# Performance work log

Hardware: AMD Instinct MI355X
Metric: run time of the kernel (lower is better)

## Reference

```python
import jax, jax.numpy as jnp
import numpy as np
import math

EPS = 1e-6
KP = -1.0  # Poincare ball curvature (c=1 -> kappa=-1)
KS = 1.0   # stereographic sphere projection (c=1 -> kappa=+1)

def _n(x):
    return jnp.sqrt(jnp.sum(x * x, -1, keepdims=True) + 1e-15)

def tan_k(u, k):
    if k < 0:
        return jnp.tanh(u)
    return jnp.tan(jnp.clip(u, -1.47079, 1.47079))

def artan_k(u, k):
    if k < 0:
        return jnp.arctanh(jnp.clip(u, -1 + 1e-5, 1 - 1e-5))
    return jnp.arctan(u)

def proj(x, k):
    if k < 0:
        n = _n(x)
        m = 1.0 - 1e-4
        return jnp.where(n > m, x * (m / n), x)
    return x

def expmap0(u, k):
    n = _n(u)
    return proj(tan_k(n, k) * u / n, k)

def logmap0(y, k):
    n = _n(y)
    return artan_k(n, k) * y / n

def _safe_den(d):
    return jnp.where(d >= 0, jnp.maximum(d, EPS), jnp.minimum(d, -EPS))

def mobius_add(x, y, k):
    x2 = jnp.sum(x * x, -1, keepdims=True)
    y2 = jnp.sum(y * y, -1, keepdims=True)
    xy = jnp.sum(x * y, -1, keepdims=True)
    num = (1 - 2 * k * xy - k * y2) * x + (1 + k * x2) * y
    den = 1 - 2 * k * xy + k * k * x2 * y2
    return proj(num / _safe_den(den), k)

def mobius_pw_mul(w, x, k):
    wx = w * x
    nx = _n(x)
    nwx = _n(wx)
    return proj(tan_k(nwx / nx * artan_k(nx, k), k) * wx / nwx, k)

def mobius_smul(r, x, k):
    n = _n(x)
    return proj(tan_k(r * artan_k(n, k), k) * x / n, k)

def wmid(xs, k, axis, w=None):
    lam = 2.0 / (1.0 + k * jnp.sum(xs * xs, -1, keepdims=True))
    if w is None:
        w = jnp.ones_like(lam)
    num = jnp.sum(w * lam * xs, axis=axis)
    den = jnp.abs(jnp.sum(w * (lam - 1.0), axis=axis))
    return mobius_smul(0.5, num / jnp.maximum(den, EPS), k)

def slin(x, W, b, k=None):
    if k is None:
        return x @ W.T + b
    return expmap0(logmap0(x, k) @ W.T + b, k)

def dist(x, y, k):
    return 2.0 * artan_k(_n(mobius_add(-x, y, k))[..., 0], k)

def hyp_attn(kk, q, v, k):
    # kk, v: [N,K,h]; q: [N,h]
    sc = -dist(q[:, None, :], kk, k)              # [N,K]
    a = jax.nn.softmax(sc, axis=1)[..., None]
    return wmid(v, k, axis=1, w=a)

def euc_attn(kk, q, v):
    sc = jnp.einsum('nkh,nh->nk', kk, q) / math.sqrt(kk.shape[-1])
    a = jax.nn.softmax(sc, axis=1)
    return jnp.einsum('nk,nkh->nh', a, v)


def _forward(x, h1, c1, h2, c2, h3, c3, del_t, iou1, iou2, iou3,
             Wq_w, Wq_b, Wc_w, Wc_b, Uf_w, Uf_b, Up_w, Up_b,
             Uiou_w, Uiou_b, d, nbr):
    sg, th = jax.nn.sigmoid, jnp.tanh
    # mailbox gather (message_func + DGL mailbox), [N,K,h]
    mh1, mh2, mh3 = h1[nbr], h2[nbr], h3[nbr]
    mc1, mc2, mc3 = c1[nbr], c2[nbr], c3[nbr]
    g_t = (d / (del_t[nbr] + 1.0))[..., None]      # [N,K,1]

    x_1p = slin(expmap0(x, KP), Wq_w, Wq_b, KP)
    x_1s = slin(expmap0(x, KS), Wq_w, Wq_b, KS)
    x_1e = slin(x, Wq_w, Wq_b)

    s1 = logmap0(sg(slin(mh1, Up_w, Up_b, KP)), KP)
    s2 = logmap0(sg(slin(mh2, Up_w, Up_b, KS)), KS)
    s3 = sg(slin(mh3, Up_w, Up_b))

    ht1p = mobius_pw_mul(s1, mh1, KP)
    ht2p = mobius_pw_mul(s2, expmap0(logmap0(mh2, KS), KP), KP)
    ht3p = mobius_pw_mul(s3, expmap0(mh3, KP), KP)
    h_1p = 3.0 * wmid(jnp.stack([ht1p, ht2p, ht3p]), KP, axis=0)

    ht1s = mobius_pw_mul(s1, expmap0(logmap0(mh1, KP), KS), KP)
    ht2s = mobius_pw_mul(s2, mh2, KS)
    ht3s = mobius_pw_mul(s3, expmap0(mh3, KS), KS)
    h_1s = 3.0 * wmid(jnp.stack([ht1s, ht2s, ht3s]), KP, axis=0)

    ht1e = logmap0(mobius_pw_mul(s1, mh1, KP), KP)
    ht2e = logmap0(mobius_pw_mul(s2, mh2, KS), KS)
    h_1e = ht1e + ht2e + s3 * mh3

    h_tildp = hyp_attn(h_1p, x_1p, h_1p, KP)
    h_tilds = hyp_attn(h_1s, x_1s, h_1s, KS)
    h_tilde = euc_attn(h_1e, x_1e, h_1e)

    # Poincare cell path
    csk_p = expmap0(th(logmap0(slin(mc1, Wc_w, Wc_b, KP), KP)), KP)
    ckt_p = mobius_add(mobius_add(-csk_p, mc1, KP), mobius_pw_mul(csk_p, g_t, KP), KP)
    f_p = sg(logmap0(slin(mh1, Uf_w, Uf_b, KP), KP))
    c_1 = wmid(mobius_pw_mul(f_p, ckt_p, KP), KP, axis=1)

    # Sphere cell path
    csk_s = expmap0(th(logmap0(slin(mc2, Wc_w, Wc_b, KS), KS)), KS)
    ckt_s = mobius_add(mobius_add(-csk_s, mc2, KS), mobius_pw_mul(csk_s, g_t, KS), KS)
    f_s = sg(logmap0(slin(mh2, Uf_w, Uf_b, KS), KS))
    c_2 = wmid(mobius_pw_mul(f_s, ckt_s, KS), KS, axis=1)

    # Euclidean cell path
    csk_e = th(slin(mc3, Wc_w, Wc_b))
    ckt_e = mc3 - csk_e + csk_e * g_t
    f_e = sg(slin(mh3, Uf_w, Uf_b))
    c_3 = jnp.sum(f_e * ckt_e, 1)

    niou1 = mobius_add(iou1, slin(h_tildp, Uiou_w, Uiou_b, KP), KP)
    niou2 = mobius_add(iou2, slin(h_tilds, Uiou_w, Uiou_b, KS), KS)
    niou3 = iou3 + slin(h_tilde, Uiou_w, Uiou_b)

    # apply_node_func
    i_p, o_p, u_p = jnp.split(niou1, 3, axis=1)
    i_p, o_p, u_p = sg(logmap0(i_p, KP)), sg(logmap0(o_p, KP)), th(logmap0(u_p, KP))
    i_s, o_s, u_s = jnp.split(niou2, 3, axis=1)
    i_s, o_s, u_s = sg(logmap0(i_s, KS)), sg(logmap0(o_s, KS)), th(logmap0(u_s, KS))
    i_e, o_e, u_e = jnp.split(niou3, 3, axis=1)
    i_e, o_e, u_e = sg(i_e), sg(o_e), th(u_e)

    nc1 = mobius_add(mobius_pw_mul(i_p, u_p, KP), c_1, KP)
    nc2 = mobius_add(mobius_pw_mul(i_s, u_s, KS), c_2, KS)
    nc3 = i_e * u_e + c_3
    nh1 = mobius_pw_mul(o_p, th(logmap0(nc1, KP)), KP)
    nh2 = mobius_pw_mul(o_s, th(logmap0(nc2, KS)), KS)
    nh3 = o_e * th(nc3)
    return jnp.stack([nh1, nc1, nh2, nc2, nh3, nc3])  # [6,N,h]


def setup_inputs() -> dict:
    N, K, H, X = 8192, 8, 128, 128
    key = jax.random.key(0)
    ks = jax.random.split(key, 24)
    def rn(i, shape, sc=0.05):
        return sc * jax.random.normal(ks[i], shape, jnp.float32)
    return dict(
        x=rn(0, (N, X)), h1=rn(1, (N, H)), c1=rn(2, (N, H)),
        h2=rn(3, (N, H)), c2=rn(4, (N, H)), h3=rn(5, (N, H)), c3=rn(6, (N, H)),
        del_t=jax.random.uniform(ks[7], (N,), jnp.float32),
        iou1=rn(8, (N, 3 * H)), iou2=rn(9, (N, 3 * H)), iou3=rn(10, (N, 3 * H)),
        Wq_w=rn(11, (H, X)), Wq_b=rn(12, (H,), 0.01),
        Wc_w=rn(13, (H, H)), Wc_b=rn(14, (H,), 0.01),
        Uf_w=rn(15, (H, H)), Uf_b=rn(16, (H,), 0.01),
        Up_w=rn(17, (H, H)), Up_b=rn(18, (H,), 0.01),
        Uiou_w=rn(19, (3 * H, H)), Uiou_b=rn(20, (3 * H,), 0.01),
        d=jnp.asarray(60.0, jnp.float32),
        nbr=jax.random.randint(ks[21], (N, K), 0, N),
    )


def reference(x, h1, c1, h2, c2, h3, c3, del_t, iou1, iou2, iou3,
              Wq_w, Wq_b, Wc_w, Wc_b, Uf_w, Uf_b, Up_w, Up_b,
              Uiou_w, Uiou_b, d, nbr):
    return _forward(x, h1, c1, h2, c2, h3, c3, del_t, iou1, iou2, iou3,
                    Wq_w, Wq_b, Wc_w, Wc_b, Uf_w, Uf_b, Up_w, Up_b,
                    Uiou_w, Uiou_b, d, nbr)
```

## Files before the change

### kernel.cpp

```cpp
#include <hip/hip_runtime.h>
#include <math.h>

#define HD 128
#define NNODE 8192
#define KNBR 8
#define NHS ((size_t)NNODE*(size_t)HD)

#define EPSF 1e-6f
#define PMX 0.9999f
#define ATHC (1.0f-1e-5f)
#define TANC 1.47079f

typedef unsigned short u16;
typedef unsigned int u32;
typedef __attribute__((ext_vector_type(8))) short short8;
typedef __attribute__((ext_vector_type(4))) float f32x4;

static __device__ __forceinline__ float frcp(float x){ return __builtin_amdgcn_rcpf(x); }
static __device__ __forceinline__ float fdiv(float a,float b){ return a*__builtin_amdgcn_rcpf(b); }
static __device__ __forceinline__ float fsqrt(float x){ return __builtin_amdgcn_sqrtf(x); }
static __device__ __forceinline__ float fexp(float x){ return __builtin_amdgcn_exp2f(x*1.4426950408889634f); }
static __device__ __forceinline__ float flog(float x){ return __builtin_amdgcn_logf(x)*0.6931471805599453f; }
static __device__ __forceinline__ float ftanh(float x){
  float ax = fabsf(x);
// ... 83 lines not shown
}

__global__ __launch_bounds__(256) void k_pre(
    const float* __restrict__ x, const float* __restrict__ h1,
    const float* __restrict__ h2, const float* __restrict__ c1,
    const float* __restrict__ c2, const float* __restrict__ h3,
    const float* __restrict__ c3, float* __restrict__ ws)
{
  int row = blockIdx.x*4 + (threadIdx.x>>6);
  int l = threadIdx.x & 63;
  size_t i0 = (size_t)row*HD + l, i1 = i0 + 64;
  float xa=x[i0], xb=x[i1];
  float h1a=h1[i0], h1b=h1[i1];
  float h2a=h2[i0], h2b=h2[i1];
  float c1a=c1[i0], c1b=c1[i1];
  float c2a=c2[i0], c2b=c2[i1];
  float h3a=h3[i0], h3b=h3[i1];
  float c3a=c3[i0], c3b=c3[i1];
  float xsq = wred(xa*xa+xb*xb);
  float h1sq = wred(h1a*h1a+h1b*h1b);
  float h2sq = wred(h2a*h2a+h2b*h2b);
  float c1sq = wred(c1a*c1a+c1b*c1b);
  float c2sq = wred(c2a*c2a+c2b*c2b);
  size_t p0 = (size_t)row*HD + l, p1 = p0 + 64;
#define WRSPLIT(R, va, vb) { \
    u16* hp = (u16*)(ws + (size_t)(R)*NHS); u16* lp2 = hp + NHS; \
    split2(va, &hp[p0], &lp2[p0]); split2(vb, &hp[p1], &lp2[p1]); }
  float nx = fsqrt(xsq+1e-15f);
  {
    float t = ftanh(nx);
    float f = fminf(t,PMX)*frcp(nx);
    float ny = fsqrt(f*f*xsq + 1e-15f);
    float g = fatanh(ny)*frcp(ny) * f;
    WRSPLIT(0, g*xa, g*xb)
  }
  {
    float t = ftan(nx);
    float f = t*frcp(nx);
    float ny = fsqrt(f*f*xsq + 1e-15f);
    float g = fatan(ny)*frcp(ny) * f;
    WRSPLIT(1, g*xa, g*xb)
  }
  WRSPLIT(2, xa, xb)
  { float n=fsqrt(h1sq+1e-15f); float g=fatanh(n)*frcp(n); WRSPLIT(3, g*h1a, g*h1b) }
  { float n=fsqrt(h2sq+1e-15f); float g=fatan(n)*frcp(n);  WRSPLIT(4, g*h2a, g*h2b) }
  WRSPLIT(5, h3a, h3b)
  { float n=fsqrt(c1sq+1e-15f); float g=fatanh(n)*frcp(n); WRSPLIT(6, g*c1a, g*c1b) }
  { float n=fsqrt(c2sq+1e-15f); float g=fatan(n)*frcp(n);  WRSPLIT(7, g*c2a, g*c2b) }
  WRSPLIT(8, c3a, c3b)
#undef WRSPLIT
}

enum { P_ID=0, P_EXP_P, P_EXP_S, P_SIG, P_TANH, P_SIG_LOG_P, P_SIG_LOG_S,
       P_LOGSIG_P, P_LOGSIG_S, P_TANH_EXP_P, P_TANH_EXP_S };

struct JobM { const u16* Ah; const u16* Al; const u16* Wh; const u16* Wl;
              const float* b; float* out; int pitch; int post; };
struct JobTabM { JobM j[12]; };

#define GITERS 4

__global__ __launch_bounds__(256) void k_gemmM(JobTabM tab){
  JobM jb = tab.j[blockIdx.y];
  __shared__ u16 Wlds[2*8*4*64*8];
  const int tid = threadIdx.x;
  for(int c = tid; c < 4096; c += 256){
    int lane_ = c & 63;
    int kk    = (c>>6)&3;
    int t     = (c>>8)&7;
    int plane = (c>>11)&1;
    const u16* src = (plane ? jb.Wl : jb.Wh)
                   + (size_t)(t*16 + (lane_&15))*128 + (lane_>>4)*8 + kk*32;
    *(uint4*)&Wlds[(size_t)c*8] = *(const uint4*)src;
  }
  const int lane = tid & 63;
  const int wave = tid >> 6;
  const int nn = lane & 15, quad = lane >> 4;
  float bias[8];
#pragma unroll
  for(int t=0;t<8;t++) bias[t] = jb.b[t*16+nn];
  __syncthreads();
#pragma unroll
  for(int it=0; it<GITERS; it++){
    const int row0 = (blockIdx.x*GITERS + it)*64 + wave*16;
    const u16* Ah = jb.Ah + (size_t)(row0+nn)*128 + quad*8;
    const u16* Al = jb.Al + (size_t)(row0+nn)*128 + quad*8;
    f32x4 acc[8];
#pragma unroll
    for(int t=0;t<8;t++) acc[t] = (f32x4){0.f,0.f,0.f,0.f};
#pragma unroll
    for(int kk=0;kk<4;kk++){
      short8 ah = *(const short8*)(Ah + kk*32);
      short8 al = *(const short8*)(Al + kk*32);
#pragma unroll
      for(int t=0;t<8;t++){
        short8 wh = *(const short8*)&Wlds[(((0*8 + t)*4 + kk)*64 + lane)*8];
        short8 wl = *(const short8*)&Wlds[(((1*8 + t)*4 + kk)*64 + lane)*8];
        acc[t] = __builtin_amdgcn_mfma_f32_16x16x32_bf16(ah, wh, acc[t], 0,0,0);
        acc[t] = __builtin_amdgcn_mfma_f32_16x16x32_bf16(al, wh, acc[t], 0,0,0);
        acc[t] = __builtin_amdgcn_mfma_f32_16x16x32_bf16(ah, wl, acc[t], 0,0,0);
      }
    }
#pragma unroll
    for(int r=0;r<4;r++){
      float v[8];
#pragma unroll
      for(int t=0;t<8;t++) v[t] = acc[t][r] + bias[t];
      float s2 = 0.f;
#pragma unroll
      for(int t=0;t<8;t++) s2 += v[t]*v[t];
      float nraw = hred16(s2);
      switch(jb.post){
        case P_ID: break;
        case P_EXP_P: {
          float n=fsqrt(nraw+1e-15f); float tt=ftanh(n); float f=fminf(tt,PMX)*frcp(n);
          for(int t=0;t<8;t++) v[t]*=f;
        } break;
        case P_EXP_S: {
          float n=fsqrt(nraw+1e-15f); float f=ftan(n)*frcp(n);
          for(int t=0;t<8;t++) v[t]*=f;
        } break;
        case P_SIG:
          for(int t=0;t<8;t++) v[t]=sigm(v[t]);
          break;
        case P_TANH:
          for(int t=0;t<8;t++) v[t]=ftanh(v[t]);
          break;
        case P_SIG_LOG_P: {
          float n=fsqrt(nraw+1e-15f); float tt=ftanh(n); float f=fminf(tt,PMX)*frcp(n);
          float z[8]; float zs=0.f;
          for(int t=0;t<8;t++){ z[t]=sigm(f*v[t]); zs+=z[t]*z[t]; }
          float zr=hred16(zs);
          float zn=fsqrt(zr+1e-15f);
          float g=fatanh(zn)*frcp(zn);
          for(int t=0;t<8;t++) v[t]=g*z[t];
        } break;
        case P_SIG_LOG_S: {
          float n=fsqrt(nraw+1e-15f); float f=ftan(n)*frcp(n);
          float z[8]; float zs=0.f;
          for(int t=0;t<8;t++){ z[t]=sigm(f*v[t]); zs+=z[t]*z[t]; }
          float zr=hred16(zs);
          float zn=fsqrt(zr+1e-15f);
          float g=fatan(zn)*frcp(zn);
          for(int t=0;t<8;t++) v[t]=g*z[t];
        } break;
        case P_LOGSIG_P: {
          float n=fsqrt(nraw+1e-15f); float tt=ftanh(n); float f=fminf(tt,PMX)*frcp(n);
          float ny=fsqrt(f*f*nraw+1e-15f);
          float g=fatanh(ny)*frcp(ny)*f;
          for(int t=0;t<8;t++) v[t]=sigm(g*v[t]);
        } break;
        case P_LOGSIG_S: {
          float n=fsqrt(nraw+1e-15f); float f=ftan(n)*frcp(n);
          float ny=fsqrt(f*f*nraw+1e-15f);
          float g=fatan(ny)*frcp(ny)*f;
          for(int t=0;t<8;t++) v[t]=sigm(g*v[t]);
        } break;
        case P_TANH_EXP_P: {
          float n=fsqrt(nraw+1e-15f); float tt=ftanh(n); float f=fminf(tt,PMX)*frcp(n);
          float ny=fsqrt(f*f*nraw+1e-15f);
          float g=fatanh(ny)*frcp(ny)*f;
          float T[8]; float Ts=0.f;
          for(int t=0;t<8;t++){ T[t]=ftanh(g*v[t]); Ts+=T[t]*T[t]; }
          float Tr=hred16(Ts);
          float Tn=fsqrt(Tr+1e-15f);
          float t2=ftanh(Tn); float f2=fminf(t2,PMX)*frcp(Tn);
          for(int t=0;t<8;t++) v[t]=f2*T[t];
        } break;
        case P_TANH_EXP_S: {
          float n=fsqrt(nraw+1e-15f); float f=ftan(n)*frcp(n);
          float ny=fsqrt(f*f*nraw+1e-15f);
          float g=fatan(ny)*frcp(ny)*f;
          float T[8]; float Ts=0.f;
          for(int t=0;t<8;t++){ T[t]=ftanh(g*v[t]); Ts+=T[t]*T[t]; }
          float Tr=hred16(Ts);
          float Tn=fsqrt(Tr+1e-15f);
          float f2=ftan(Tn)*frcp(Tn);
          for(int t=0;t<8;t++) v[t]=f2*T[t];
        } break;
      }
      float* orow = jb.out + (size_t)(row0 + quad*4 + r)*jb.pitch + nn;
#pragma unroll
      for(int t=0;t<8;t++) orow[t*16] = v[t];
    }
  }
}

__global__ __launch_bounds__(256) void k_phaseB(
  const float* __restrict__ h1,const float* __restrict__ h2,const float* __restrict__ h3,
  const float* __restrict__ c1,const float* __restrict__ c2,const float* __restrict__ c3,
  const float* __restrict__ del_t, const float* __restrict__ dsc,
  float* __restrict__ ws)
{
  const float* S1 = ws+9*NHS;  const float* S2 = ws+10*NHS; const float* S3 = ws+11*NHS;
  const float* F1 = ws+12*NHS; const float* F2 = ws+13*NHS; const float* F3 = ws+14*NHS;
  const float* Q1 = ws+15*NHS; const float* Q2 = ws+16*NHS; const float* Q3 = ws+17*NHS;
  float* H1P = ws+21*NHS; float* H1S = ws+22*NHS; float* H1E = ws+23*NHS;
  float* V1 = ws+24*NHS;  float* V2 = ws+25*NHS;  float* V3 = ws+26*NHS;
  float* y2p = ws+SCOFF; float* y2s = y2p+8192; float* d1 = y2p+16384; float* d2 = y2p+24576;

  int j = blockIdx.x*4 + (threadIdx.x>>6);
  int l = threadIdx.x&63;
  size_t i0 = (size_t)j*HD+l, i1 = i0+64;
  float h1a=h1[i0],h1b=h1[i1], h2a=h2[i0],h2b=h2[i1], h3a=h3[i0],h3b=h3[i1];
  float c1a=c1[i0],c1b=c1[i1], c2a=c2[i0],c2b=c2[i1], c3a=c3[i0],c3b=c3[i1];
  float s1a=S1[i0],s1b=S1[i1], s2a=S2[i0],s2b=S2[i1], s3a=S3[i0],s3b=S3[i1];
  float f1a=F1[i0],f1b=F1[i1], f2a=F2[i0],f2b=F2[i1], f3a=F3[i0],f3b=F3[i1];
  float q1a=Q1[i0],q1b=Q1[i1], q2a=Q2[i0],q2b=Q2[i1], q3a=Q3[i0],q3b=Q3[i1];
  float g = fdiv(dsc[0], del_t[j]+1.0f);

  float h1sq = wred(h1a*h1a+h1b*h1b); float n1 = fsqrt(h1sq+1e-15f);
  float h2sq = wred(h2a*h2a+h2b*h2b); float n2 = fsqrt(h2sq+1e-15f);
  float h3sq = wred(h3a*h3a+h3b*h3b); float n3 = fsqrt(h3sq+1e-15f);
  float w1a=s1a*h1a, w1b=s1b*h1b;
  float w2a=s2a*h2a, w2b=s2b*h2b;
  float w3a=s3a*h3a, w3b=s3b*h3b;
  float w1sq = wred(w1a*w1a+w1b*w1b); float nw1 = fsqrt(w1sq+1e-15f);
  float w2sq = wred(w2a*w2a+w2b*w2b); float nw2 = fsqrt(w2sq+1e-15f);
  float w3sq = wred(w3a*w3a+w3b*w3b); float nw3 = fsqrt(w3sq+1e-15f);

  float t1 = ftanh(nw1*frcp(n1) * fatanh(n1));
  float fp1 = fminf(t1,PMX)*frcp(nw1); float np1 = fminf(t1,PMX);
  float nu2 = fatan(n2);
  float ne2 = fminf(ftanh(nu2),PMX);
  float t2 = ftanh(nw2*frcp(n2) * fatanh(ne2));
  float fp2 = fminf(t2,PMX)*frcp(nw2); float np2 = fminf(t2,PMX);
  float ne3 = fminf(ftanh(n3),PMX);
  float t3 = ftanh(nw3*frcp(n3) * fatanh(ne3));
  float fp3 = fminf(t3,PMX)*frcp(nw3); float np3 = fminf(t3,PMX);
  {
    float lamA = 2.0f*frcp(1.0f-np1*np1), lamB = 2.0f*frcp(1.0f-np2*np2), lamC = 2.0f*frcp(1.0f-np3*np3);
    float dn = frcp(fmaxf(fabsf(lamA+lamB+lamC-3.0f), EPSF));
    float va = (lamA*fp1*w1a + lamB*fp2*w2a + lamC*fp3*w3a)*dn;
    float vb = (lamA*fp1*w1b + lamB*fp2*w2b + lamC*fp3*w3b)*dn;
    float vsq = wred(va*va+vb*vb); float nv = fsqrt(vsq+1e-15f);
    float tt = ftanh(0.5f*fatanh(nv)); float ff = 3.0f*fminf(tt,PMX)*frcp(nv);
    H1P[i0]=ff*va; H1P[i1]=ff*vb;
    if(l==0) y2p[j] = ff*ff*vsq;
  }
  float t2s, fs2;
  {
    float nx1s = ftan(fatanh(n1));
    float t1s = ftanh(nw1*frcp(n1) * fatanh(nx1s));
    float fs1 = fminf(t1s,PMX)*frcp(nw1); float ns1 = fminf(t1s,PMX);
    t2s = ftan(nw2*frcp(n2) * fatan(n2));
    fs2 = t2s*frcp(nw2);
    float nx3s = ftan(n3);
    float t3s = ftan(nw3*frcp(n3) * fatan(nx3s));
    float fs3 = t3s*frcp(nw3);
    float lA = 2.0f*frcp(1.0f-ns1*ns1), lB = 2.0f*frcp(1.0f-t2s*t2s), lC = 2.0f*frcp(1.0f-t3s*t3s);
    float dns = frcp(fmaxf(fabsf(lA+lB+lC-3.0f), EPSF));
    float vsa = (lA*fs1*w1a + lB*fs2*w2a + lC*fs3*w3a)*dns;
    float vsb = (lA*fs1*w1b + lB*fs2*w2b + lC*fs3*w3b)*dns;
    float vssq = wred(vsa*vsa+vsb*vsb); float nvs = fsqrt(vssq+1e-15f);
    float tts = ftan(0.5f*fatan(nvs)); float ffs = 3.0f*tts*frcp(nvs);
    H1S[i0]=ffs*vsa; H1S[i1]=ffs*vsb;
    if(l==0) y2s[j] = ffs*ffs*vssq;
  }
  {
    float ne1 = fsqrt(fp1*fp1*w1sq + 1e-15f);
    float ge1 = fatanh(ne1)*frcp(ne1);
    float n2s_ = fsqrt(fs2*fs2*w2sq + 1e-15f);
    float ge2 = fatan(n2s_)*frcp(n2s_);
    H1E[i0] = ge1*fp1*w1a + ge2*fs2*w2a + s3a*h3a;
    H1E[i1] = ge1*fp1*w1b + ge2*fs2*w2b + s3b*h3b;
  }
  float ng = fsqrt(g*g+1e-15f);
  {
    float q1sq = wred(q1a*q1a+q1b*q1b);
    float c1rs = wred(c1a*c1a+c1b*c1b);
    float dq1 = wred(q1a*c1a+q1b*c1b);
    float xy = -dq1;
    float aa = 1.0f+2.0f*xy+c1rs, bb = 1.0f-q1sq;
    float dd = frcp(safeden(1.0f+2.0f*xy+q1sq*c1rs));
    float m1a = (aa*(-q1a)+bb*c1a)*dd, m1b = (aa*(-q1b)+bb*c1b)*dd;
    float m1sq = (aa*aa*q1sq + 2.0f*aa*bb*xy + bb*bb*c1rs)*dd*dd;
    float mdq = (-aa*q1sq + bb*dq1)*dd;
    { float nm = fsqrt(m1sq+1e-15f);
      if(nm>PMX){ float sc=PMX*frcp(nm); m1a*=sc; m1b*=sc; m1sq*=sc*sc; mdq*=sc; } }
    float nwg = fsqrt(g*g*q1sq+1e-15f);
    float tg = ftanh(nwg*frcp(ng) * fatanh(ng));
    float fX = fminf(tg,PMX)*frcp(nwg) * g;
    float X2sq = fX*fX*q1sq;
    float xy2 = fX*mdq;
    float a2 = 1.0f+2.0f*xy2+X2sq, b2 = 1.0f-m1sq;
    float d2d = frcp(safeden(1.0f+2.0f*xy2+m1sq*X2sq));
    float ka = (a2*m1a + b2*fX*q1a)*d2d, kb = (a2*m1b + b2*fX*q1b)*d2d;
    float ksq = (a2*a2*m1sq + 2.0f*a2*b2*xy2 + b2*b2*X2sq)*d2d*d2d;
    { float nk0 = fsqrt(ksq+1e-15f);
      if(nk0>PMX){ float sc=PMX*frcp(nk0); ka*=sc; kb*=sc; ksq*=sc*sc; } }
    float nk = fsqrt(ksq+1e-15f);
    float wfa = f1a*ka, wfb = f1b*kb;
    float wfsq = wred(wfa*wfa+wfb*wfb); float nwf = fsqrt(wfsq+1e-15f);
    float tu = ftanh(nwf*frcp(nk) * fatanh(nk));
    float fu = fminf(tu,PMX)*frcp(nwf);
    float u1sq = fu*fu*wfsq;
    float lam = 2.0f*frcp(1.0f-u1sq);
    V1[i0]=lam*fu*wfa; V1[i1]=lam*fu*wfb;
    if(l==0) d1[j]=lam-1.0f;
  }
  {
    float q2sq = wred(q2a*q2a+q2b*q2b);
    float c2rs = wred(c2a*c2a+c2b*c2b);
    float dq2 = wred(q2a*c2a+q2b*c2b);
    float xy = -dq2;
    float aa = 1.0f-2.0f*xy-c2rs, bb = 1.0f+q2sq;
    float dd = frcp(safeden(1.0f-2.0f*xy+q2sq*c2rs));
    float ma = (aa*(-q2a)+bb*c2a)*dd, mb = (aa*(-q2b)+bb*c2b)*dd;
    float msq = (aa*aa*q2sq + 2.0f*aa*bb*xy + bb*bb*c2rs)*dd*dd;
    float mdq = (-aa*q2sq + bb*dq2)*dd;
    float nwg = fsqrt(g*g*q2sq+1e-15f);
    float tg = ftan(nwg*frcp(ng) * fatan(ng));
    float fX = tg*frcp(nwg) * g;
    float X2sq = fX*fX*q2sq;
    float xy2 = fX*mdq;
    float a2 = 1.0f-2.0f*xy2-X2sq, b2 = 1.0f+msq;
    float d2d = frcp(safeden(1.0f-2.0f*xy2+msq*X2sq));
    float ka = (a2*ma + b2*fX*q2a)*d2d, kb = (a2*mb + b2*fX*q2b)*d2d;
    float ksq = (a2*a2*msq + 2.0f*a2*b2*xy2 + b2*b2*X2sq)*d2d*d2d;
    float nk = fsqrt(ksq+1e-15f);
    float wfa = f2a*ka, wfb = f2b*kb;
    float wfsq = wred(wfa*wfa+wfb*wfb); float nwf = fsqrt(wfsq+1e-15f);
    float tu = ftan(nwf*frcp(nk) * fatan(nk));
    float fu = tu*frcp(nwf);
    float u2sq = fu*fu*wfsq;
    float lam = 2.0f*frcp(1.0f+u2sq);
    V2[i0]=lam*fu*wfa; V2[i1]=lam*fu*wfb;
    if(l==0) d2[j]=lam-1.0f;
  }
  {
    float kea = c3a + q3a*(g-1.0f), keb = c3b + q3b*(g-1.0f);
    V3[i0]=f3a*kea; V3[i1]=f3b*keb;
  }
}

__global__ __launch_bounds__(256) void k_attn(
  const int* __restrict__ nbr, float* __restrict__ ws)
{
  const float* XP = ws+18*NHS; const float* XS = ws+19*NHS; const float* XE = ws+20*NHS;
  const float* H1P = ws+21*NHS; const float* H1S = ws+22*NHS; const float* H1E = ws+23*NHS;
  const float* V1 = ws+24*NHS; const float* V2 = ws+25*NHS; const float* V3 = ws+26*NHS;
  u16* LPh = (u16*)(ws+9*NHS);  u16* LPl = LPh + NHS;
  u16* LSh = (u16*)(ws+10*NHS); u16* LSl = LSh + NHS;
  u16* LEh = (u16*)(ws+11*NHS); u16* LEl = LEh + NHS;
  float* C1o = ws+12*NHS; float* C2o = ws+13*NHS; float* C3o = ws+14*NHS;
  const float* y2p = ws+SCOFF; const float* y2s = y2p+8192;
  const float* d1 = y2p+16384; const float* d2 = y2p+24576;
  float* c1n2 = (float*)(y2p+32768); float* c2n2 = (float*)(y2p+40960);

  int n = blockIdx.x*4 + (threadIdx.x>>6);
  int l = threadIdx.x&63;
  size_t i0 = (size_t)n*HD+l, i1 = i0+64;
  float XPa=XP[i0], XPb=XP[i1];
  float XSa=XS[i0], XSb=XS[i1];
  float XEa=XE[i0], XEb=XE[i1];
  float x2p = wred(XPa*XPa+XPb*XPb);
  float x2s = wred(XSa*XSa+XSb*XSb);
  float HPa[8],HPb[8],HSa[8],HSb[8],HEa[8],HEb[8],y2pk[8],y2sk[8];
  float scp[8],scs[8],sce[8];
  float v1a=0,v1b=0,v2a=0,v2b=0,v3a=0,v3b=0,ds1=0,ds2=0;
  const float rs = 0.08838834764831845f;
#pragma unroll
  for(int k=0;k<8;k++){
    int j = nbr[n*KNBR+k];
    size_t j0 = (size_t)j*HD+l, j1 = j0+64;
    HPa[k]=H1P[j0]; HPb[k]=H1P[j1];
    HSa[k]=H1S[j0]; HSb[k]=H1S[j1];
    HEa[k]=H1E[j0]; HEb[k]=H1E[j1];
    y2pk[k]=y2p[j]; y2sk[k]=y2s[j];
    v1a+=V1[j0]; v1b+=V1[j1];
    v2a+=V2[j0]; v2b+=V2[j1];
    v3a+=V3[j0]; v3b+=V3[j1];
    ds1+=d1[j]; ds2+=d2[j];
    float dp = wred(XPa*HPa[k]+XPb*HPb[k]);
    {
      float xy=-dp, y2=y2pk[k];
      float aa=1.0f+2.0f*xy+y2, bb=1.0f-x2p;
      float dd=frcp(safeden(1.0f+2.0f*xy+x2p*y2));
      float nsq=(aa*aa*x2p+2.0f*aa*bb*xy+bb*bb*y2)*dd*dd;
      float nn=fminf(fsqrt(nsq+1e-15f),PMX);
      scp[k] = -2.0f*fatanh(nn);
    }
    float dsv = wred(XSa*HSa[k]+XSb*HSb[k]);
    {
      float xy=-dsv, y2=y2sk[k];
      float aa=1.0f-2.0f*xy-y2, bb=1.0f+x2s;
      float dd=frcp(safeden(1.0f-2.0f*xy+x2s*y2));
      float nsq=(aa*aa*x2s+2.0f*aa*bb*xy+bb*bb*y2)*dd*dd;
      float nn=fsqrt(nsq+1e-15f);
      scs[k] = -2.0f*fatan(nn);
    }
    sce[k] = wred(XEa*HEa[k]+XEb*HEb[k])*rs;
  }
  {
    float mx=scp[0];
#pragma unroll
    for(int k=1;k<8;k++) mx=fmaxf(mx,scp[k]);
    float a[8]; float s=0;
#pragma unroll
    for(int k=0;k<8;k++){ a[k]=fexp(scp[k]-mx); s+=a[k]; }
    float inv=frcp(s);
    float na=0,nb=0,de=0;
#pragma unroll
    for(int k=0;k<8;k++){
      float lam = 2.0f*frcp(1.0f-y2pk[k]); float w=a[k]*inv;
      na+=w*lam*HPa[k]; nb+=w*lam*HPb[k]; de+=w*(lam-1.0f);
    }
    de = frcp(fmaxf(fabsf(de),EPSF));
    na*=de; nb*=de;
    float vsq=wred(na*na+nb*nb); float nv=fsqrt(vsq+1e-15f);
    float tt=ftanh(0.5f*fatanh(nv)); float f=fminf(tt,PMX)*frcp(nv);
    float ha=f*na, hb=f*nb;
    float hn=fsqrt(f*f*vsq+1e-15f);
    float gl=fatanh(hn)*frcp(hn);
    split2(gl*ha, &LPh[i0], &LPl[i0]); split2(gl*hb, &LPh[i1], &LPl[i1]);
  }
  {
    float mx=scs[0];
#pragma unroll
    for(int k=1;k<8;k++) mx=fmaxf(mx,scs[k]);
    float a[8]; float s=0;
#pragma unroll
    for(int k=0;k<8;k++){ a[k]=fexp(scs[k]-mx); s+=a[k]; }
    float inv=frcp(s);
    float na=0,nb=0,de=0;
#pragma unroll
    for(int k=0;k<8;k++){
      float lam = 2.0f*frcp(1.0f+y2sk[k]); float w=a[k]*inv;
      na+=w*lam*HSa[k]; nb+=w*lam*HSb[k]; de+=w*(lam-1.0f);
    }
    de = frcp(fmaxf(fabsf(de),EPSF));
    na*=de; nb*=de;
    float vsq=wred(na*na+nb*nb); float nv=fsqrt(vsq+1e-15f);
    float tt=ftan(0.5f*fatan(nv)); float f=tt*frcp(nv);
    float ha=f*na, hb=f*nb;
    float hn=fsqrt(f*f*vsq+1e-15f);
    float gl=fatan(hn)*frcp(hn);
    split2(gl*ha, &LSh[i0], &LSl[i0]); split2(gl*hb, &LSh[i1], &LSl[i1]);
  }
  {
    float mx=sce[0];
#pragma unroll
    for(int k=1;k<8;k++) mx=fmaxf(mx,sce[k]);
    float a[8]; float s=0;
#pragma unroll
    for(int k=0;k<8;k++){ a[k]=fexp(sce[k]-mx); s+=a[k]; }
    float inv=frcp(s);
    float ha=0,hb=0;
#pragma unroll
    for(int k=0;k<8;k++){ float w=a[k]*inv; ha+=w*HEa[k]; hb+=w*HEb[k]; }
    split2(ha, &LEh[i0], &LEl[i0]); split2(hb, &LEh[i1], &LEl[i1]);
  }
  {
    float de=frcp(fmaxf(fabsf(ds1),EPSF));
    float na=v1a*de, nb=v1b*de;
// ... 110 lines not shown
    float ncsq=(a3*a3*p2+2.0f*a3*b3*xyc+b3*b3*y2c)*d3*d3;
    float nl=fsqrt(ncsq+1e-15f);
    float gL=fatan(nl)*frcp(nl);
    float T0=ftanh(gL*nc0), T1=ftanh(gL*nc1_);
    float tsq=wred(T0*T0+T1*T1); float nT=fsqrt(tsq+1e-15f);
    float wo0=op0*T0, wo1=op1*T1;
    float osq=wred(wo0*wo0+wo1*wo1); float nwo=fsqrt(osq+1e-15f);
    float tH=ftan(nwo*frcp(nT)*fatan(nT)); float fH=tH*frcp(nwo);
    out[2*NHS + b128]=fH*wo0; out[2*NHS + b128+64]=fH*wo1;
    out[3*NHS + b128]=nc0;    out[3*NHS + b128+64]=nc1_;
  }
  {
    float Y[6], I[6];
#pragma unroll
    for(int r=0;r<6;r++){ Y[r]=YE[b384+64*r]; I[r]=iou3[b384+64*r]; }
    float n0=I[0]+Y[0], n1=I[1]+Y[1];
    float n2=I[2]+Y[2], n3=I[3]+Y[3];
    float n4=I[4]+Y[4], n5=I[5]+Y[5];
    float ie0=sigm(n0), ie1=sigm(n1);
    float oe0=sigm(n2), oe1=sigm(n3);
    float ue0=ftanh(n4), ue1=ftanh(n5);
    float ca=C3v[b128], cb=C3v[b128+64];
    float nc0=ie0*ue0+ca, nc1_=ie1*ue1+cb;
    out[4*NHS + b128]=oe0*ftanh(nc0); out[4*NHS + b128+64]=oe1*ftanh(nc1_);
    out[5*NHS + b128]=nc0;            out[5*NHS + b128+64]=nc1_;
  }
}

extern "C" void kernel_launch(void* const* d_in, const int* in_sizes, int n_in,
                              void* d_out, int out_size, void* d_ws, size_t ws_size,
                              hipStream_t stream)
{
  const float* x     = (const float*)d_in[0];
  const float* h1    = (const float*)d_in[1];
  const float* c1    = (const float*)d_in[2];
  const float* h2    = (const float*)d_in[3];
  const float* c2    = (const float*)d_in[4];
  const float* h3    = (const float*)d_in[5];
  const float* c3    = (const float*)d_in[6];
  const float* del_t = (const float*)d_in[7];
  const float* iou1  = (const float*)d_in[8];
  const float* iou2  = (const float*)d_in[9];
  const float* iou3  = (const float*)d_in[10];
  const float* Wq_w  = (const float*)d_in[11];
  const float* Wq_b  = (const float*)d_in[12];
  const float* Wc_w  = (const float*)d_in[13];
  const float* Wc_b  = (const float*)d_in[14];
  const float* Uf_w  = (const float*)d_in[15];
  const float* Uf_b  = (const float*)d_in[16];
  const float* Up_w  = (const float*)d_in[17];
  const float* Up_b  = (const float*)d_in[18];
  const float* Uiou_w= (const float*)d_in[19];
  const float* Uiou_b= (const float*)d_in[20];
  const float* dsc   = (const float*)d_in[21];
  const int*   nbr   = (const int*)d_in[22];
  float* out = (float*)d_out;
  float* ws  = (float*)d_ws;

  k_wsplit<<<112,256,0,stream>>>(Wq_w,Wc_w,Uf_w,Up_w,Uiou_w,ws);
  k_pre<<<2048,256,0,stream>>>(x,h1,h2,c1,c2,h3,c3,ws);

  u16* WH = (u16*)(ws + WOFF);
  u16* WL = WH + NW;
  const u16* Wqh = WH;           const u16* Wql = WL;
  const u16* Wch = WH + 16384;   const u16* Wcl = WL + 16384;
  const u16* Ufh = WH + 32768;   const u16* Ufl = WL + 32768;
  const u16* Uph = WH + 49152;   const u16* Upl = WL + 49152;
  const u16* UIh = WH + 65536;   const u16* UIl = WL + 65536;
#define APLANE(R) ((const u16*)(ws + (size_t)(R)*NHS)), ((const u16*)(ws + (size_t)(R)*NHS) + NHS)

  JobTabM A{};
  A.j[0]  = { APLANE(0), Wqh, Wql, Wq_b, ws+18*NHS, 128, P_EXP_P };
  A.j[1]  = { APLANE(1), Wqh, Wql, Wq_b, ws+19*NHS, 128, P_EXP_S };
  A.j[2]  = { APLANE(2), Wqh, Wql, Wq_b, ws+20*NHS, 128, P_ID };
  A.j[3]  = { APLANE(3), Uph, Upl, Up_b, ws+9*NHS,  128, P_SIG_LOG_P };
  A.j[4]  = { APLANE(4), Uph, Upl, Up_b, ws+10*NHS, 128, P_SIG_LOG_S };
  A.j[5]  = { APLANE(5), Uph, Upl, Up_b, ws+11*NHS, 128, P_SIG };
  A.j[6]  = { APLANE(3), Ufh, Ufl, Uf_b, ws+12*NHS, 128, P_LOGSIG_P };
  A.j[7]  = { APLANE(4), Ufh, Ufl, Uf_b, ws+13*NHS, 128, P_LOGSIG_S };
  A.j[8]  = { APLANE(5), Ufh, Ufl, Uf_b, ws+14*NHS, 128, P_SIG };
  A.j[9]  = { APLANE(6), Wch, Wcl, Wc_b, ws+15*NHS, 128, P_TANH_EXP_P };
  A.j[10] = { APLANE(7), Wch, Wcl, Wc_b, ws+16*NHS, 128, P_TANH_EXP_S };
  A.j[11] = { APLANE(8), Wch, Wcl, Wc_b, ws+17*NHS, 128, P_TANH };
  k_gemmM<<<dim3(NNODE/(GITERS*64),12),256,0,stream>>>(A);

  k_phaseB<<<2048,256,0,stream>>>(h1,h2,h3,c1,c2,c3,del_t,dsc,ws);
  k_attn<<<2048,256,0,stream>>>(nbr,ws);

  JobTabM B{};
  for(int ct=0; ct<3; ct++){
    B.j[0*3+ct] = { APLANE(9),  UIh + ct*16384, UIl + ct*16384, Uiou_b + ct*128, ws+0*NHS + ct*128, 384, P_ID };
    B.j[1*3+ct] = { APLANE(10), UIh + ct*16384, UIl + ct*16384, Uiou_b + ct*128, ws+3*NHS + ct*128, 384, P_ID };
    B.j[2*3+ct] = { APLANE(11), UIh + ct*16384, UIl + ct*16384, Uiou_b + ct*128, ws+6*NHS + ct*128, 384, P_ID };
  }
  k_gemmM<<<dim3(NNODE/(GITERS*64),9),256,0,stream>>>(B);

  k_final<<<2048,256,0,stream>>>(iou1,iou2,iou3,ws,out);
}
```

Baseline: 282.0 us.

## Store gathered neighbor tensors in bf16 and widen GEMM tiles to 32 rows per wave

The intermediate H1P/H1S/H1E and V1/V2/V3 tensors, which the attention kernel gathers per neighbor, are now stored as bf16 instead of fp32. This halves the random-gather traffic in the attention kernel. Separately, each wave of the GEMM now computes two 16-row sub-tiles, so every LDS weight fragment read feeds two sets of MFMAs, and the grid is halved to match. The bf16 storage lowers precision on these intermediates, and the doubled accumulators raise register pressure.

```diff
diff --git a/kernel.cpp b/kernel.cpp
--- a/kernel.cpp
+++ b/kernel.cpp
@@ -189,106 +189,118 @@
   __syncthreads();
 #pragma unroll
   for(int it=0; it<GITERS; it++){
-    const int row0 = (blockIdx.x*GITERS + it)*64 + wave*16;
-    const u16* Ah = jb.Ah + (size_t)(row0+nn)*128 + quad*8;
-    const u16* Al = jb.Al + (size_t)(row0+nn)*128 + quad*8;
-    f32x4 acc[8];
-#pragma unroll
-    for(int t=0;t<8;t++) acc[t] = (f32x4){0.f,0.f,0.f,0.f};
+    const int row0 = (blockIdx.x*GITERS + it)*128 + wave*32;
+    const u16* Ah0 = jb.Ah + (size_t)(row0+nn)*128 + quad*8;
+    const u16* Al0 = jb.Al + (size_t)(row0+nn)*128 + quad*8;
+    f32x4 acc[2][8];
+#pragma unroll
+    for(int s=0;s<2;s++)
+#pragma unroll
+      for(int t=0;t<8;t++) acc[s][t] = (f32x4){0.f,0.f,0.f,0.f};
 #pragma unroll
     for(int kk=0;kk<4;kk++){
-      short8 ah = *(const short8*)(Ah + kk*32);
-      short8 al = *(const short8*)(Al + kk*32);
+      short8 ah0 = *(const short8*)(Ah0 + kk*32);
+      short8 al0 = *(const short8*)(Al0 + kk*32);
+      short8 ah1 = *(const short8*)(Ah0 + 16*128 + kk*32);
+      short8 al1 = *(const short8*)(Al0 + 16*128 + kk*32);
 #pragma unroll
       for(int t=0;t<8;t++){
-        short8 wh = *(const short8*)&Wlds[(((0*8 + t)*4 + kk)*64 + lane)*8];
-        short8 wl = *(const short8*)&Wlds[(((1*8 + t)*4 + kk)*64 + lane)*8];
-        acc[t] = __builtin_amdgcn_mfma_f32_16x16x32_bf16(ah, wh, acc[t], 0,0,0);
-        acc[t] = __builtin_amdgcn_mfma_f32_16x16x32_bf16(al, wh, acc[t], 0,0,0);
-        acc[t] = __builtin_amdgcn_mfma_f32_16x16x32_bf16(ah, wl, acc[t], 0,0,0);
+        short8 wh = *(const short8*)&Wlds[((t*4 + kk)*64 + lane)*8];
+        short8 wl = *(const short8*)&Wlds[((2048/8 + t*4*64) + kk*64 + lane)*8];
+        wl = *(const short8*)&Wlds[(((8 + t)*4 + kk)*64 + lane)*8];
+        acc[0][t] = __builtin_amdgcn_mfma_f32_16x16x32_bf16(ah0, wh, acc[0][t], 0,0,0);
+        acc[0][t] = __builtin_amdgcn_mfma_f32_16x16x32_bf16(al0, wh, acc[0][t], 0,0,0);
+        acc[0][t] = __builtin_amdgcn_mfma_f32_16x16x32_bf16(ah0, wl, acc[0][t], 0,0,0);
+        acc[1][t] = __builtin_amdgcn_mfma_f32_16x16x32_bf16(ah1, wh, acc[1][t], 0,0,0);
+        acc[1][t] = __builtin_amdgcn_mfma_f32_16x16x32_bf16(al1, wh, acc[1][t], 0,0,0);
+        acc[1][t] = __builtin_amdgcn_mfma_f32_16x16x32_bf16(ah1, wl, acc[1][t], 0,0,0);
       }
     }
 #pragma unroll
-    for(int r=0;r<4;r++){
-      float v[8];
-#pragma unroll
-      for(int t=0;t<8;t++) v[t] = acc[t][r] + bias[t];
-      float s2 = 0.f;
-#pragma unroll
-      for(int t=0;t<8;t++) s2 += v[t]*v[t];
-      float nraw = hred16(s2);
-      switch(jb.post){
-        case P_ID: break;
-        case P_EXP_P: {
-          float n=fsqrt(nraw+1e-15f); float tt=ftanh(n); float f=fminf(tt,PMX)*frcp(n);
-          for(int t=0;t<8;t++) v[t]*=f;
-        } break;
-        case P_EXP_S: {
-          float n=fsqrt(nraw+1e-15f); float f=ftan(n)*frcp(n);
-          for(int t=0;t<8;t++) v[t]*=f;
-        } break;
-        case P_SIG:
-          for(int t=0;t<8;t++) v[t]=sigm(v[t]);
-          break;
-        case P_TANH:
-          for(int t=0;t<8;t++) v[t]=ftanh(v[t]);
-          break;
-        case P_SIG_LOG_P: {
-          float n=fsqrt(nraw+1e-15f); float tt=ftanh(n); float f=fminf(tt,PMX)*frcp(n);
-          float z[8]; float zs=0.f;
-          for(int t=0;t<8;t++){ z[t]=sigm(f*v[t]); zs+=z[t]*z[t]; }
-          float zr=hred16(zs);
-          float zn=fsqrt(zr+1e-15f);
-          float g=fatanh(zn)*frcp(zn);
-          for(int t=0;t<8;t++) v[t]=g*z[t];
-        } break;
-        case P_SIG_LOG_S: {
-          float n=fsqrt(nraw+1e-15f); float f=ftan(n)*frcp(n);
-          float z[8]; float zs=0.f;
-          for(int t=0;t<8;t++){ z[t]=sigm(f*v[t]); zs+=z[t]*z[t]; }
-          float zr=hred16(zs);
-          float zn=fsqrt(zr+1e-15f);
-          float g=fatan(zn)*frcp(zn);
-          for(int t=0;t<8;t++) v[t]=g*z[t];
-        } break;
-        case P_LOGSIG_P: {
-          float n=fsqrt(nraw+1e-15f); float tt=ftanh(n); float f=fminf(tt,PMX)*frcp(n);
-          float ny=fsqrt(f*f*nraw+1e-15f);
-          float g=fatanh(ny)*frcp(ny)*f;
-          for(int t=0;t<8;t++) v[t]=sigm(g*v[t]);
-        } break;
-        case P_LOGSIG_S: {
-          float n=fsqrt(nraw+1e-15f); float f=ftan(n)*frcp(n);
-          float ny=fsqrt(f*f*nraw+1e-15f);
-          float g=fatan(ny)*frcp(ny)*f;
-          for(int t=0;t<8;t++) v[t]=sigm(g*v[t]);
-        } break;
-        case P_TANH_EXP_P: {
-          float n=fsqrt(nraw+1e-15f); float tt=ftanh(n); float f=fminf(tt,PMX)*frcp(n);
-          float ny=fsqrt(f*f*nraw+1e-15f);
-          float g=fatanh(ny)*frcp(ny)*f;
-          float T[8]; float Ts=0.f;
-          for(int t=0;t<8;t++){ T[t]=ftanh(g*v[t]); Ts+=T[t]*T[t]; }
-          float Tr=hred16(Ts);
-          float Tn=fsqrt(Tr+1e-15f);
-          float t2=ftanh(Tn); float f2=fminf(t2,PMX)*frcp(Tn);
-          for(int t=0;t<8;t++) v[t]=f2*T[t];
-        } break;
-        case P_TANH_EXP_S: {
-          float n=fsqrt(nraw+1e-15f); float f=ftan(n)*frcp(n);
-          float ny=fsqrt(f*f*nraw+1e-15f);
-          float g=fatan(ny)*frcp(ny)*f;
-          float T[8]; float Ts=0.f;
-          for(int t=0;t<8;t++){ T[t]=ftanh(g*v[t]); Ts+=T[t]*T[t]; }
-          float Tr=hred16(Ts);
-          float Tn=fsqrt(Tr+1e-15f);
-          float f2=ftan(Tn)*frcp(Tn);
-          for(int t=0;t<8;t++) v[t]=f2*T[t];
-        } break;
+    for(int s=0;s<2;s++){
+      const int rbase = row0 + s*16;
+#pragma unroll
+      for(int r=0;r<4;r++){
+        float v[8];
+#pragma unroll
+        for(int t=0;t<8;t++) v[t] = acc[s][t][r] + bias[t];
+        float s2 = 0.f;
+#pragma unroll
+        for(int t=0;t<8;t++) s2 += v[t]*v[t];
+        float nraw = hred16(s2);
+        switch(jb.post){
+          case P_ID: break;
+          case P_EXP_P: {
+            float n=fsqrt(nraw+1e-15f); float tt=ftanh(n); float f=fminf(tt,PMX)*frcp(n);
+            for(int t=0;t<8;t++) v[t]*=f;
+          } break;
+          case P_EXP_S: {
+            float n=fsqrt(nraw+1e-15f); float f=ftan(n)*frcp(n);
+            for(int t=0;t<8;t++) v[t]*=f;
+          } break;
+          case P_SIG:
+            for(int t=0;t<8;t++) v[t]=sigm(v[t]);
+            break;
+          case P_TANH:
+            for(int t=0;t<8;t++) v[t]=ftanh(v[t]);
+            break;
+          case P_SIG_LOG_P: {
+            float n=fsqrt(nraw+1e-15f); float tt=ftanh(n); float f=fminf(tt,PMX)*frcp(n);
+            float z[8]; float zs=0.f;
+            for(int t=0;t<8;t++){ z[t]=sigm(f*v[t]); zs+=z[t]*z[t]; }
+            float zr=hred16(zs);
+            float zn=fsqrt(zr+1e-15f);
+            float g=fatanh(zn)*frcp(zn);
+            for(int t=0;t<8;t++) v[t]=g*z[t];
+          } break;
+          case P_SIG_LOG_S: {
+            float n=fsqrt(nraw+1e-15f); float f=ftan(n)*frcp(n);
+            float z[8]; float zs=0.f;
+            for(int t=0;t<8;t++){ z[t]=sigm(f*v[t]); zs+=z[t]*z[t]; }
+            float zr=hred16(zs);
+            float zn=fsqrt(zr+1e-15f);
+            float g=fatan(zn)*frcp(zn);
+            for(int t=0;t<8;t++) v[t]=g*z[t];
+          } break;
+          case P_LOGSIG_P: {
+            float n=fsqrt(nraw+1e-15f); float tt=ftanh(n); float f=fminf(tt,PMX)*frcp(n);
+            float ny=fsqrt(f*f*nraw+1e-15f);
+            float g=fatanh(ny)*frcp(ny)*f;
+            for(int t=0;t<8;t++) v[t]=sigm(g*v[t]);
+          } break;
+          case P_LOGSIG_S: {
+            float n=fsqrt(nraw+1e-15f); float f=ftan(n)*frcp(n);
+            float ny=fsqrt(f*f*nraw+1e-15f);
+            float g=fatan(ny)*frcp(ny)*f;
+            for(int t=0;t<8;t++) v[t]=sigm(g*v[t]);
+          } break;
+          case P_TANH_EXP_P: {
+            float n=fsqrt(nraw+1e-15f); float tt=ftanh(n); float f=fminf(tt,PMX)*frcp(n);
+            float ny=fsqrt(f*f*nraw+1e-15f);
+            float g=fatanh(ny)*frcp(ny)*f;
+            float T[8]; float Ts=0.f;
+            for(int t=0;t<8;t++){ T[t]=ftanh(g*v[t]); Ts+=T[t]*T[t]; }
+            float Tr=hred16(Ts);
+            float Tn=fsqrt(Tr+1e-15f);
+            float t2=ftanh(Tn); float f2=fminf(t2,PMX)*frcp(Tn);
+            for(int t=0;t<8;t++) v[t]=f2*T[t];
+          } break;
+          case P_TANH_EXP_S: {
+            float n=fsqrt(nraw+1e-15f); float f=ftan(n)*frcp(n);
+            float ny=fsqrt(f*f*nraw+1e-15f);
+            float g=fatan(ny)*frcp(ny)*f;
+            float T[8]; float Ts=0.f;
+            for(int t=0;t<8;t++){ T[t]=ftanh(g*v[t]); Ts+=T[t]*T[t]; }
+            float Tr=hred16(Ts);
+            float Tn=fsqrt(Tr+1e-15f);
+            float f2=ftan(Tn)*frcp(Tn);
+            for(int t=0;t<8;t++) v[t]=f2*T[t];
+          } break;
+        }
+        float* orow = jb.out + (size_t)(rbase + quad*4 + r)*jb.pitch + nn;
+#pragma unroll
+        for(int t=0;t<8;t++) orow[t*16] = v[t];
       }
-      float* orow = jb.out + (size_t)(row0 + quad*4 + r)*jb.pitch + nn;
-#pragma unroll
-      for(int t=0;t<8;t++) orow[t*16] = v[t];
     }
   }
 }
@@ -302,8 +314,8 @@
   const float* S1 = ws+9*NHS;  const float* S2 = ws+10*NHS; const float* S3 = ws+11*NHS;
   const float* F1 = ws+12*NHS; const float* F2 = ws+13*NHS; const float* F3 = ws+14*NHS;
   const float* Q1 = ws+15*NHS; const float* Q2 = ws+16*NHS; const float* Q3 = ws+17*NHS;
-  float* H1P = ws+21*NHS; float* H1S = ws+22*NHS; float* H1E = ws+23*NHS;
-  float* V1 = ws+24*NHS;  float* V2 = ws+25*NHS;  float* V3 = ws+26*NHS;
+  u16* H1P = (u16*)(ws+21*NHS); u16* H1S = (u16*)(ws+22*NHS); u16* H1E = (u16*)(ws+23*NHS);
+  u16* V1 = (u16*)(ws+24*NHS);  u16* V2 = (u16*)(ws+25*NHS);  u16* V3 = (u16*)(ws+26*NHS);
   float* y2p = ws+SCOFF; float* y2s = y2p+8192; float* d1 = y2p+16384; float* d2 = y2p+24576;
 
   int j = blockIdx.x*4 + (threadIdx.x>>6);
@@ -342,7 +354,7 @@
     float vb = (lamA*fp1*w1b + lamB*fp2*w2b + lamC*fp3*w3b)*dn;
     float vsq = wred(va*va+vb*vb); float nv = fsqrt(vsq+1e-15f);
     float tt = ftanh(0.5f*fatanh(nv)); float ff = 3.0f*fminf(tt,PMX)*frcp(nv);
-    H1P[i0]=ff*va; H1P[i1]=ff*vb;
+    H1P[i0]=f2bf(ff*va); H1P[i1]=f2bf(ff*vb);
     if(l==0) y2p[j] = ff*ff*vsq;
   }
   float t2s, fs2;
@@ -361,7 +373,7 @@
     float vsb = (lA*fs1*w1b + lB*fs2*w2b + lC*fs3*w3b)*dns;
     float vssq = wred(vsa*vsa+vsb*vsb); float nvs = fsqrt(vssq+1e-15f);
     float tts = ftan(0.5f*fatan(nvs)); float ffs = 3.0f*tts*frcp(nvs);
-    H1S[i0]=ffs*vsa; H1S[i1]=ffs*vsb;
+    H1S[i0]=f2bf(ffs*vsa); H1S[i1]=f2bf(ffs*vsb);
     if(l==0) y2s[j] = ffs*ffs*vssq;
   }
   {
@@ -369,8 +381,8 @@
     float ge1 = fatanh(ne1)*frcp(ne1);
     float n2s_ = fsqrt(fs2*fs2*w2sq + 1e-15f);
     float ge2 = fatan(n2s_)*frcp(n2s_);
-    H1E[i0] = ge1*fp1*w1a + ge2*fs2*w2a + s3a*h3a;
-    H1E[i1] = ge1*fp1*w1b + ge2*fs2*w2b + s3b*h3b;
+    H1E[i0] = f2bf(ge1*fp1*w1a + ge2*fs2*w2a + s3a*h3a);
+    H1E[i1] = f2bf(ge1*fp1*w1b + ge2*fs2*w2b + s3b*h3b);
   }
   float ng = fsqrt(g*g+1e-15f);
   {
@@ -403,7 +415,7 @@
     float fu = fminf(tu,PMX)*frcp(nwf);
     float u1sq = fu*fu*wfsq;
     float lam = 2.0f*frcp(1.0f-u1sq);
-    V1[i0]=lam*fu*wfa; V1[i1]=lam*fu*wfb;
+    V1[i0]=f2bf(lam*fu*wfa); V1[i1]=f2bf(lam*fu*wfb);
     if(l==0) d1[j]=lam-1.0f;
   }
   {
@@ -432,12 +444,12 @@
     float fu = tu*frcp(nwf);
     float u2sq = fu*fu*wfsq;
     float lam = 2.0f*frcp(1.0f+u2sq);
-    V2[i0]=lam*fu*wfa; V2[i1]=lam*fu*wfb;
+    V2[i0]=f2bf(lam*fu*wfa); V2[i1]=f2bf(lam*fu*wfb);
     if(l==0) d2[j]=lam-1.0f;
   }
   {
     float kea = c3a + q3a*(g-1.0f), keb = c3b + q3b*(g-1.0f);
-    V3[i0]=f3a*kea; V3[i1]=f3b*keb;
+    V3[i0]=f2bf(f3a*kea); V3[i1]=f2bf(f3b*keb);
   }
 }
 
@@ -445,8 +457,10 @@
   const int* __restrict__ nbr, float* __restrict__ ws)
 {
   const float* XP = ws+18*NHS; const float* XS = ws+19*NHS; const float* XE = ws+20*NHS;
-  const float* H1P = ws+21*NHS; const float* H1S = ws+22*NHS; const float* H1E = ws+23*NHS;
-  const float* V1 = ws+24*NHS; const float* V2 = ws+25*NHS; const float* V3 = ws+26*NHS;
+  const u16* H1P = (const u16*)(ws+21*NHS); const u16* H1S = (const u16*)(ws+22*NHS);
+  const u16* H1E = (const u16*)(ws+23*NHS);
+  const u16* V1 = (const u16*)(ws+24*NHS); const u16* V2 = (const u16*)(ws+25*NHS);
+  const u16* V3 = (const u16*)(ws+26*NHS);
   u16* LPh = (u16*)(ws+9*NHS);  u16* LPl = LPh + NHS;
   u16* LSh = (u16*)(ws+10*NHS); u16* LSl = LSh + NHS;
   u16* LEh = (u16*)(ws+11*NHS); u16* LEl = LEh + NHS;
@@ -471,13 +485,13 @@
   for(int k=0;k<8;k++){
     int j = nbr[n*KNBR+k];
     size_t j0 = (size_t)j*HD+l, j1 = j0+64;
-    HPa[k]=H1P[j0]; HPb[k]=H1P[j1];
-    HSa[k]=H1S[j0]; HSb[k]=H1S[j1];
-    HEa[k]=H1E[j0]; HEb[k]=H1E[j1];
+    HPa[k]=bf2f(H1P[j0]); HPb[k]=bf2f(H1P[j1]);
+    HSa[k]=bf2f(H1S[j0]); HSb[k]=bf2f(H1S[j1]);
+    HEa[k]=bf2f(H1E[j0]); HEb[k]=bf2f(H1E[j1]);
     y2pk[k]=y2p[j]; y2sk[k]=y2s[j];
-    v1a+=V1[j0]; v1b+=V1[j1];
-    v2a+=V2[j0]; v2b+=V2[j1];
-    v3a+=V3[j0]; v3b+=V3[j1];
+    v1a+=bf2f(V1[j0]); v1b+=bf2f(V1[j1]);
+    v2a+=bf2f(V2[j0]); v2b+=bf2f(V2[j1]);
+    v3a+=bf2f(V3[j0]); v3b+=bf2f(V3[j1]);
     ds1+=d1[j]; ds2+=d2[j];
     float dp = wred(XPa*HPa[k]+XPb*HPb[k]);
     {
@@ -754,7 +768,7 @@
   A.j[9]  = { APLANE(6), Wch, Wcl, Wc_b, ws+15*NHS, 128, P_TANH_EXP_P };
   A.j[10] = { APLANE(7), Wch, Wcl, Wc_b, ws+16*NHS, 128, P_TANH_EXP_S };
   A.j[11] = { APLANE(8), Wch, Wcl, Wc_b, ws+17*NHS, 128, P_TANH };
-  k_gemmM<<<dim3(NNODE/(GITERS*64),12),256,0,stream>>>(A);
+  k_gemmM<<<dim3(NNODE/(GITERS*128),12),256,0,stream>>>(A);
 
   k_phaseB<<<2048,256,0,stream>>>(h1,h2,h3,c1,c2,c3,del_t,dsc,ws);
   k_attn<<<2048,256,0,stream>>>(nbr,ws);
@@ -765,7 +779,7 @@
     B.j[1*3+ct] = { APLANE(10), UIh + ct*16384, UIl + ct*16384, Uiou_b + ct*128, ws+3*NHS + ct*128, 384, P_ID };
     B.j[2*3+ct] = { APLANE(11), UIh + ct*16384, UIl + ct*16384, Uiou_b + ct*128, ws+6*NHS + ct*128, 384, P_ID };
   }
-  k_gemmM<<<dim3(NNODE/(GITERS*64),9),256,0,stream>>>(B);
+  k_gemmM<<<dim3(NNODE/(GITERS*128),9),256,0,stream>>>(B);
 
   k_final<<<2048,256,0,stream>>>(iou1,iou2,iou3,ws,out);
 }
```

Measured after the change: 394.0 us. 39.7% more time.
